# Kernel tuning notes

Measured on AMD Instinct MI355X. Metric: run time of the kernel, lower is better.

The kernel has to match this reference:

```python
import jax, jax.numpy as jnp
import numpy as np

N_NODES = 100000
N_EDGES = 1600000
IN_F = 256
OUT_F = 128


def setup_inputs() -> dict:
    key = jax.random.key(0)
    k1, k2, k3, k4, k5 = jax.random.split(key, 5)
    x = jax.random.normal(k1, (N_NODES, IN_F), dtype=jnp.float32)
    edge_rows = jax.random.randint(k2, (N_EDGES,), 0, N_NODES, dtype=jnp.int32)
    edge_cols = jax.random.randint(k3, (N_EDGES,), 0, N_NODES, dtype=jnp.int32)
    edge_vals = jax.random.uniform(k4, (N_EDGES,), dtype=jnp.float32)
    # glorot init for weight, zeros for bias (matches reset_parameters)
    limit = float(np.sqrt(6.0 / (IN_F + OUT_F)))
    weight = jax.random.uniform(k5, (IN_F, OUT_F), dtype=jnp.float32,
                                minval=-limit, maxval=limit)
    bias = jnp.zeros((OUT_F,), dtype=jnp.float32)
    return {"x": x, "edge_rows": edge_rows, "edge_cols": edge_cols,
            "edge_vals": edge_vals, "weight": weight, "bias": bias}


def reference(x, edge_rows, edge_cols, edge_vals, weight, bias):
    # dense projection: [N, in] @ [in, out] -> [N, out]
    h = x @ weight
    # spmm(adj, h): out[r] = sum_{edges e with row r} vals[e] * h[col[e]]
    msgs = edge_vals[:, None] * h[edge_cols]          # [E, out]
    agg = jax.ops.segment_sum(msgs, edge_rows, num_segments=N_NODES)
    return agg + bias
```

## Files before the change

kernel.cpp:

```cpp
#include <hip/hip_runtime.h>


typedef __attribute__((ext_vector_type(8))) short short8;
typedef __attribute__((ext_vector_type(4))) float floatx4;
typedef __attribute__((ext_vector_type(2))) int intv2;

#define WT_K 264
#define GM_NODES 128
#define BSHIFT 6
#define BROWS 64
#define CAP 192
#define CSH 4
#define OVFCAP 65536
#define XCC_GETREG_IMM 6164

static __device__ __forceinline__ uint f2bf(float x) {
  uint u = __float_as_uint(x);
  return (u + 0x7fffu + ((u >> 16) & 1u)) >> 16;
}

__global__ __launch_bounds__(256) void conv_w(const float* __restrict__ w,
                                              ushort* __restrict__ wt,
                                              int* __restrict__ cursors,
                                              int n_ints) {
  const int f = blockIdx.x;
  const int k = threadIdx.x;
  wt[f * WT_K + k] = (ushort)f2bf(w[k * 128 + f]);
  for (int i = blockIdx.x * 256 + threadIdx.x; i < n_ints; i += 128 * 256)
    cursors[i] = 0;
}

__global__ __launch_bounds__(256) void gemm_mfma(const float* __restrict__ x,
                                                 const ushort* __restrict__ wt,
                                                 ushort* __restrict__ h,
                                                 int n_nodes) {
  __shared__ ushort lw[128 * WT_K];
  __shared__ ushort xa[GM_NODES * 40];
  const int t = threadIdx.x;
  const int lane = t & 63;
  const int wq = t >> 6;
  const int quad = lane >> 4;
  const int l15 = lane & 15;
  const int row0 = blockIdx.x * GM_NODES;

  {
    const uint4* src = (const uint4*)wt;
    uint4* dst = (uint4*)lw;
    for (int i = t; i < (128 * WT_K * 2) / 16; i += 256) dst[i] = src[i];
  }

  floatx4 acc[2][8];
#pragma unroll
  for (int nt = 0; nt < 2; ++nt)
#pragma unroll
    for (int mt = 0; mt < 8; ++mt) acc[nt][mt] = (floatx4){0.f, 0.f, 0.f, 0.f};

  float4 cur[4];
#pragma unroll
  for (int i = 0; i < 4; ++i) {
    const int idx = i * 256 + t;
    const int row = idx >> 3, kq = idx & 7;
    const int gr = row0 + row;
    cur[i] = (gr < n_nodes) ? *(const float4*)&x[(size_t)gr * 256 + kq * 4]
                            : make_float4(0.f, 0.f, 0.f, 0.f);
  }

  for (int kc = 0; kc < 8; ++kc) {
#pragma unroll
    for (int i = 0; i < 4; ++i) {
      const int idx = i * 256 + t;
      const int row = idx >> 3, kq = idx & 7;
      uint2 p;
      p.x = f2bf(cur[i].x) | (f2bf(cur[i].y) << 16);
      p.y = f2bf(cur[i].z) | (f2bf(cur[i].w) << 16);
      *(uint2*)&xa[row * 40 + kq * 4] = p;
    }
    __syncthreads();

    float4 nxt[4];
    if (kc < 7) {
#pragma unroll
      for (int i = 0; i < 4; ++i) {
        const int idx = i * 256 + t;
        const int row = idx >> 3, kq = idx & 7;
        const int gr = row0 + row;
        nxt[i] = (gr < n_nodes)
                     ? *(const float4*)&x[(size_t)gr * 256 + (kc + 1) * 32 + kq * 4]
                     : make_float4(0.f, 0.f, 0.f, 0.f);
      }
    }

    short8 bfr[2];
    bfr[0] = *(const short8*)&xa[(wq * 32 + l15) * 40 + quad * 8];
    bfr[1] = *(const short8*)&xa[(wq * 32 + 16 + l15) * 40 + quad * 8];
#pragma unroll
    for (int mt = 0; mt < 8; ++mt) {
      const short8 afr =
          *(const short8*)&lw[(mt * 16 + l15) * WT_K + kc * 32 + quad * 8];
      acc[0][mt] = __builtin_amdgcn_mfma_f32_16x16x32_bf16(afr, bfr[0],
                                                           acc[0][mt], 0, 0, 0);
      acc[1][mt] = __builtin_amdgcn_mfma_f32_16x16x32_bf16(afr, bfr[1],
                                                           acc[1][mt], 0, 0, 0);
    }
    __syncthreads();
#pragma unroll
    for (int i = 0; i < 4; ++i) cur[i] = nxt[i];
  }

#pragma unroll
  for (int nt = 0; nt < 2; ++nt) {
    const int node = row0 + wq * 32 + nt * 16 + l15;
    if (node < n_nodes) {
#pragma unroll
      for (int mt = 0; mt < 8; ++mt) {
        uint2 p;
        p.x = f2bf(acc[nt][mt][0]) | (f2bf(acc[nt][mt][1]) << 16);
        p.y = f2bf(acc[nt][mt][2]) | (f2bf(acc[nt][mt][3]) << 16);
        *(uint2*)&h[(size_t)node * 128 + mt * 16 + quad * 4] = p;
      }
    }
  }
}

__global__ __launch_bounds__(256) void fill_xcd(
    const int* __restrict__ erows, const int* __restrict__ ecols,
    const float* __restrict__ evals, int* __restrict__ cursors,
    int2* __restrict__ bcv, int* __restrict__ ovf_cnt,
    int4* __restrict__ ovf, int n_edges, int nb) {
  const int base = blockIdx.x * 1024 + threadIdx.x;
  const int xcd = (int)(__builtin_amdgcn_s_getreg(XCC_GETREG_IMM)) & 7;
  int rr[4], cc[4];
  float vv[4];
#pragma unroll
  for (int j = 0; j < 4; ++j) {
    const int i = base + j * 256;
    if (i < n_edges) {
      rr[j] = __builtin_nontemporal_load(&erows[i]);
      cc[j] = __builtin_nontemporal_load(&ecols[i]);
      vv[j] = __builtin_nontemporal_load(&evals[i]);
    }
  }
#pragma unroll
  for (int j = 0; j < 4; ++j) {
    const int i = base + j * 256;
    if (i >= n_edges) continue;
    const int reg = xcd * nb + (rr[j] >> BSHIFT);
    const int pos = atomicAdd(&cursors[reg << CSH], 1);
    if (pos < CAP) {
      int2 p;
      p.x = cc[j] | ((rr[j] & (BROWS - 1)) << 17);
      p.y = __float_as_int(vv[j]);
      bcv[(size_t)reg * CAP + pos] = p;
    } else {
      int op = atomicAdd(ovf_cnt, 1);
      if (op < OVFCAP) {
        int4 q; q.x = rr[j]; q.y = cc[j]; q.z = __float_as_int(vv[j]); q.w = 0;
        ovf[op] = q;
      }
    }
  }
}

__global__ __launch_bounds__(256) void sort_gather(
    const ushort* __restrict__ h, const int* __restrict__ cursors,
    const int2* __restrict__ bcv, const float* __restrict__ bias,
    float* __restrict__ out, int n_nodes, int nb) {
  __shared__ int2 buf[8 * CAP];
  __shared__ int cnt[BROWS], start[BROWS], cur[BROWS];
  __shared__ int scnt[8];
  const int b = blockIdx.x;
  const int t = threadIdx.x;
  if (t < 8) scnt[t] = min(cursors[(t * nb + b) << CSH], CAP);
  if (t < BROWS) cnt[t] = 0;
  __syncthreads();

#pragma unroll
  for (int x = 0; x < 8; ++x) {
    const int n = scnt[x];
    const int2* src = &bcv[(size_t)(x * nb + b) * CAP];
    for (int i = t; i < n; i += 256) atomicAdd(&cnt[((uint)src[i].x) >> 17], 1);
  }
  __syncthreads();

  if (t < BROWS) {
    int c = cnt[t];
    int s = c;
#pragma unroll
    for (int off = 1; off < 64; off <<= 1) {
      int u = __shfl_up(s, off, 64);
      if (t >= off) s += u;
    }
    start[t] = s - c;
    cur[t] = s - c;
  }
  __syncthreads();

#pragma unroll
  for (int x = 0; x < 8; ++x) {
    const int n = scnt[x];
    const intv2* src = (const intv2*)&bcv[(size_t)(x * nb + b) * CAP];
    for (int i = t; i < n; i += 256) {
      intv2 rr = __builtin_nontemporal_load(&src[i]);
      int2 rec; rec.x = rr[0]; rec.y = rr[1];
      int pos = atomicAdd(&cur[((uint)rec.x) >> 17], 1);
      buf[pos] = rec;
    }
  }
  __syncthreads();

  const int lane = t & 63;
  const int w = t >> 6;
  const float2 bv = ((const float2*)bias)[lane];
  for (int rr = w * 16; rr < w * 16 + 16; ++rr) {
    const int node = b * BROWS + rr;
    if (node >= n_nodes) break;
    float2 acca = bv;
    float2 accb = make_float2(0.f, 0.f);
    int p = start[rr];
    const int p1 = start[rr] + cnt[rr];
    for (; p + 8 <= p1; p += 8) {
      int2 e0 = buf[p + 0];
      int2 e1 = buf[p + 1];
      int2 e2 = buf[p + 2];
      int2 e3 = buf[p + 3];
      int2 e4 = buf[p + 4];
      int2 e5 = buf[p + 5];
      int2 e6 = buf[p + 6];
      int2 e7 = buf[p + 7];
      uint u0 = ((const uint*)(h + (size_t)(e0.x & 0x1FFFF) * 128))[lane];
      uint u1 = ((const uint*)(h + (size_t)(e1.x & 0x1FFFF) * 128))[lane];
      uint u2 = ((const uint*)(h + (size_t)(e2.x & 0x1FFFF) * 128))[lane];
      uint u3 = ((const uint*)(h + (size_t)(e3.x & 0x1FFFF) * 128))[lane];
      uint u4 = ((const uint*)(h + (size_t)(e4.x & 0x1FFFF) * 128))[lane];
      uint u5 = ((const uint*)(h + (size_t)(e5.x & 0x1FFFF) * 128))[lane];
      uint u6 = ((const uint*)(h + (size_t)(e6.x & 0x1FFFF) * 128))[lane];
      uint u7 = ((const uint*)(h + (size_t)(e7.x & 0x1FFFF) * 128))[lane];
      float v0 = __int_as_float(e0.y), v1 = __int_as_float(e1.y);
      float v2 = __int_as_float(e2.y), v3 = __int_as_float(e3.y);
      float v4 = __int_as_float(e4.y), v5 = __int_as_float(e5.y);
      float v6 = __int_as_float(e6.y), v7 = __int_as_float(e7.y);
      acca.x += v0 * __uint_as_float(u0 << 16);
      acca.y += v0 * __uint_as_float(u0 & 0xffff0000u);
      accb.x += v1 * __uint_as_float(u1 << 16);
      accb.y += v1 * __uint_as_float(u1 & 0xffff0000u);
      acca.x += v2 * __uint_as_float(u2 << 16);
      acca.y += v2 * __uint_as_float(u2 & 0xffff0000u);
      accb.x += v3 * __uint_as_float(u3 << 16);
      accb.y += v3 * __uint_as_float(u3 & 0xffff0000u);
      acca.x += v4 * __uint_as_float(u4 << 16);
      acca.y += v4 * __uint_as_float(u4 & 0xffff0000u);
      accb.x += v5 * __uint_as_float(u5 << 16);
      accb.y += v5 * __uint_as_float(u5 & 0xffff0000u);
      acca.x += v6 * __uint_as_float(u6 << 16);
      acca.y += v6 * __uint_as_float(u6 & 0xffff0000u);
      accb.x += v7 * __uint_as_float(u7 << 16);
      accb.y += v7 * __uint_as_float(u7 & 0xffff0000u);
    }
    for (; p < p1; ++p) {
      int2 ev = buf[p];
      float v = __int_as_float(ev.y);
      uint u = ((const uint*)(h + (size_t)(ev.x & 0x1FFFF) * 128))[lane];
      acca.x += v * __uint_as_float(u << 16);
      acca.y += v * __uint_as_float(u & 0xffff0000u);
    }
    float2 accf;
    accf.x = acca.x + accb.x;
    accf.y = acca.y + accb.y;
    ((float2*)(out + (size_t)node * 128))[lane] = accf;
  }
}

__global__ __launch_bounds__(256) void ovf_scatter(
    const ushort* __restrict__ h, const int* __restrict__ ovf_cnt,
    const int4* __restrict__ ovf, float* __restrict__ out) {
  const int n = min(*ovf_cnt, OVFCAP);
  const int lane = threadIdx.x & 63;
  const int wid = (blockIdx.x * 256 + threadIdx.x) >> 6;
  const int nw = gridDim.x * 4;
  for (int e = wid; e < n; e += nw) {
    int4 rec = ovf[e];
    float v = __int_as_float(rec.z);
    uint u = ((const uint*)(h + (size_t)rec.y * 128))[lane];
    float* op = out + (size_t)rec.x * 128 + lane * 2;
    atomicAdd(op, v * __uint_as_float(u << 16));
    atomicAdd(op + 1, v * __uint_as_float(u & 0xffff0000u));
  }
}

__global__ __launch_bounds__(256) void init_bias(float* __restrict__ out,
                                                 const float* __restrict__ bias,
                                                 int n4) {
  int i = blockIdx.x * 256 + threadIdx.x;
  if (i < n4) {
    float4 b = ((const float4*)bias)[i & 31];
    ((float4*)out)[i] = b;
  }
}

__global__ __launch_bounds__(256) void scatter_edges(
    const ushort* __restrict__ h, const int* __restrict__ erows,
    const int* __restrict__ ecols, const float* __restrict__ evals,
    float* __restrict__ out, int n_edges) {
  int e = blockIdx.x * 4 + (threadIdx.x >> 6);
  if (e >= n_edges) return;
  int lane = threadIdx.x & 63;
  int row = erows[e];
  int col = ecols[e];
  float v = evals[e];
  uint u = ((const uint*)(h + (size_t)col * 128))[lane];
  float* op = out + (size_t)row * 128 + lane * 2;
  atomicAdd(op, v * __uint_as_float(u << 16));
  atomicAdd(op + 1, v * __uint_as_float(u & 0xffff0000u));
}

extern "C" void kernel_launch(void* const* d_in, const int* in_sizes, int n_in,
                              void* d_out, int out_size, void* d_ws, size_t ws_size,
                              hipStream_t stream) {
  const float* x     = (const float*)d_in[0];
  const int*   erows = (const int*)d_in[1];
  const int*   ecols = (const int*)d_in[2];
  const float* evals = (const float*)d_in[3];
  const float* w     = (const float*)d_in[4];
  const float* bias  = (const float*)d_in[5];
  float* out = (float*)d_out;

  const int n_nodes = in_sizes[0] / 256;
  const int n_edges = in_sizes[1];
  const int nb_buckets = (n_nodes + BROWS - 1) >> BSHIFT;
  const int nb8 = nb_buckets * 8;

  char* ws = (char*)d_ws;
  size_t off = 0;
  ushort* h  = (ushort*)(ws + off);  off += ((size_t)n_nodes * 128 * 2 + 255) & ~255ull;
  ushort* wt = (ushort*)(ws + off);  off += ((size_t)128 * WT_K * 2 + 255) & ~255ull;
  const size_t cur_ints = (((size_t)nb8) << CSH) + 16;
  int* cursors = (int*)(ws + off);   off += (cur_ints * 4 + 255) & ~255ull;
  int2* bcv    = (int2*)(ws + off);  off += ((size_t)nb8 * CAP * 8 + 255) & ~255ull;
  int4* ovf    = (int4*)(ws + off);  off += (size_t)OVFCAP * 16;
  const bool bucket_ok = (off <= ws_size) && (n_nodes <= (1 << 17));
  int* ovf_cnt = cursors + (((size_t)nb8) << CSH);

  const int zero_ints = bucket_ok ? (int)cur_ints : 0;
  conv_w<<<128, 256, 0, stream>>>(w, wt, cursors, zero_ints);
  const int gemm_blocks = (n_nodes + GM_NODES - 1) / GM_NODES;
  gemm_mfma<<<gemm_blocks, 256, 0, stream>>>(x, wt, h, n_nodes);

  if (bucket_ok) {
    const int eblocks = (n_edges + 1023) / 1024;
    fill_xcd<<<eblocks, 256, 0, stream>>>(erows, ecols, evals, cursors, bcv,
                                          ovf_cnt, ovf, n_edges, nb_buckets);
    sort_gather<<<nb_buckets, 256, 0, stream>>>(h, cursors, bcv, bias, out,
                                                n_nodes, nb_buckets);
    ovf_scatter<<<32, 256, 0, stream>>>(h, ovf_cnt, ovf, out);
  } else {
    const int n4 = out_size / 4;
    init_bias<<<(n4 + 255) / 256, 256, 0, stream>>>(out, bias, n4);
    scatter_edges<<<(n_edges + 3) / 4, 256, 0, stream>>>(h, erows, ecols, evals,
                                                         out, n_edges);
  }
}
```

Baseline: 334.6 us.

## Pre-bin edges in shared memory per block before global bucket reservation

Replaces the per-edge global atomic bucket fill, which used per-XCD bucket copies, with a block-local counting sort. Each block loads 6400 edges into LDS, histograms them by bucket, reserves one contiguous range per bucket with a single global atomic, then scatters the records. Buckets become unified, each holding up to 1280 records, so sort_gather reads one segment per bucket instead of eight. This cuts global atomic traffic heavily. In exchange it uses a large LDS footprint per block and adds tighter limits on node count.

```diff
diff --git a/kernel.cpp b/kernel.cpp
--- a/kernel.cpp
+++ b/kernel.cpp
@@ -9,10 +9,11 @@
 #define GM_NODES 128
 #define BSHIFT 6
 #define BROWS 64
-#define CAP 192
+#define CAP 1280
+#define NBMAX 1600
+#define EPB 6400
 #define CSH 4
 #define OVFCAP 65536
-#define XCC_GETREG_IMM 6164
 
 static __device__ __forceinline__ uint f2bf(float x) {
   uint u = __float_as_uint(x);
@@ -122,39 +123,82 @@
   }
 }
 
-__global__ __launch_bounds__(256) void fill_xcd(
+__global__ __launch_bounds__(256) void fill_bin(
     const int* __restrict__ erows, const int* __restrict__ ecols,
     const float* __restrict__ evals, int* __restrict__ cursors,
     int2* __restrict__ bcv, int* __restrict__ ovf_cnt,
     int4* __restrict__ ovf, int n_edges, int nb) {
-  const int base = blockIdx.x * 1024 + threadIdx.x;
-  const int xcd = (int)(__builtin_amdgcn_s_getreg(XCC_GETREG_IMM)) & 7;
-  int rr[4], cc[4];
-  float vv[4];
-#pragma unroll
-  for (int j = 0; j < 4; ++j) {
-    const int i = base + j * 256;
-    if (i < n_edges) {
-      rr[j] = __builtin_nontemporal_load(&erows[i]);
-      cc[j] = __builtin_nontemporal_load(&ecols[i]);
-      vv[j] = __builtin_nontemporal_load(&evals[i]);
-    }
-  }
-#pragma unroll
-  for (int j = 0; j < 4; ++j) {
-    const int i = base + j * 256;
-    if (i >= n_edges) continue;
-    const int reg = xcd * nb + (rr[j] >> BSHIFT);
-    const int pos = atomicAdd(&cursors[reg << CSH], 1);
+  __shared__ int2 rec[EPB];
+  __shared__ short bkt[EPB];
+  __shared__ int cnt[NBMAX], bas[NBMAX], cur[NBMAX];
+  const int t = threadIdx.x;
+  const int e0 = blockIdx.x * EPB;
+  const int n = min(EPB, n_edges - e0);
+  if (n <= 0) return;
+
+  for (int b = t; b < nb; b += 256) { cnt[b] = 0; cur[b] = 0; }
+  __syncthreads();
+
+  {
+    int i = t;
+    for (; i + 768 < n; i += 1024) {
+      int r0 = __builtin_nontemporal_load(&erows[e0 + i]);
+      int r1 = __builtin_nontemporal_load(&erows[e0 + i + 256]);
+      int r2 = __builtin_nontemporal_load(&erows[e0 + i + 512]);
+      int r3 = __builtin_nontemporal_load(&erows[e0 + i + 768]);
+      int c0 = __builtin_nontemporal_load(&ecols[e0 + i]);
+      int c1 = __builtin_nontemporal_load(&ecols[e0 + i + 256]);
+      int c2 = __builtin_nontemporal_load(&ecols[e0 + i + 512]);
+      int c3 = __builtin_nontemporal_load(&ecols[e0 + i + 768]);
+      float v0 = __builtin_nontemporal_load(&evals[e0 + i]);
+      float v1 = __builtin_nontemporal_load(&evals[e0 + i + 256]);
+      float v2 = __builtin_nontemporal_load(&evals[e0 + i + 512]);
+      float v3 = __builtin_nontemporal_load(&evals[e0 + i + 768]);
+      int2 p0; p0.x = c0 | ((r0 & (BROWS - 1)) << 17); p0.y = __float_as_int(v0);
+      int2 p1; p1.x = c1 | ((r1 & (BROWS - 1)) << 17); p1.y = __float_as_int(v1);
+      int2 p2; p2.x = c2 | ((r2 & (BROWS - 1)) << 17); p2.y = __float_as_int(v2);
+      int2 p3; p3.x = c3 | ((r3 & (BROWS - 1)) << 17); p3.y = __float_as_int(v3);
+      rec[i] = p0; rec[i + 256] = p1; rec[i + 512] = p2; rec[i + 768] = p3;
+      const int b0 = r0 >> BSHIFT, b1 = r1 >> BSHIFT;
+      const int b2 = r2 >> BSHIFT, b3 = r3 >> BSHIFT;
+      bkt[i] = (short)b0; bkt[i + 256] = (short)b1;
+      bkt[i + 512] = (short)b2; bkt[i + 768] = (short)b3;
+      atomicAdd(&cnt[b0], 1); atomicAdd(&cnt[b1], 1);
+      atomicAdd(&cnt[b2], 1); atomicAdd(&cnt[b3], 1);
+    }
+    for (; i < n; i += 256) {
+      const int r = __builtin_nontemporal_load(&erows[e0 + i]);
+      const int c = __builtin_nontemporal_load(&ecols[e0 + i]);
+      const float v = __builtin_nontemporal_load(&evals[e0 + i]);
+      int2 p; p.x = c | ((r & (BROWS - 1)) << 17); p.y = __float_as_int(v);
+      rec[i] = p;
+      const int b = r >> BSHIFT;
+      bkt[i] = (short)b;
+      atomicAdd(&cnt[b], 1);
+    }
+  }
+  __syncthreads();
+
+  for (int b = t; b < nb; b += 256) {
+    const int c = cnt[b];
+    if (c > 0) bas[b] = atomicAdd(&cursors[b << CSH], c);
+  }
+  __syncthreads();
+
+  for (int i = t; i < n; i += 256) {
+    const int b = (int)bkt[i];
+    const int loc = atomicAdd(&cur[b], 1);
+    const int pos = bas[b] + loc;
+    const int2 p = rec[i];
     if (pos < CAP) {
-      int2 p;
-      p.x = cc[j] | ((rr[j] & (BROWS - 1)) << 17);
-      p.y = __float_as_int(vv[j]);
-      bcv[(size_t)reg * CAP + pos] = p;
+      bcv[(size_t)b * CAP + pos] = p;
     } else {
       int op = atomicAdd(ovf_cnt, 1);
       if (op < OVFCAP) {
-        int4 q; q.x = rr[j]; q.y = cc[j]; q.z = __float_as_int(vv[j]); q.w = 0;
+        int4 q;
+        q.x = (b << BSHIFT) | ((p.x >> 17) & (BROWS - 1));
+        q.y = p.x & 0x1FFFF;
+        q.z = p.y; q.w = 0;
         ovf[op] = q;
       }
     }
@@ -165,21 +209,16 @@
     const ushort* __restrict__ h, const int* __restrict__ cursors,
     const int2* __restrict__ bcv, const float* __restrict__ bias,
     float* __restrict__ out, int n_nodes, int nb) {
-  __shared__ int2 buf[8 * CAP];
+  __shared__ int2 buf[CAP];
   __shared__ int cnt[BROWS], start[BROWS], cur[BROWS];
-  __shared__ int scnt[8];
   const int b = blockIdx.x;
   const int t = threadIdx.x;
-  if (t < 8) scnt[t] = min(cursors[(t * nb + b) << CSH], CAP);
+  const int nrec = min(cursors[b << CSH], CAP);
   if (t < BROWS) cnt[t] = 0;
   __syncthreads();
 
-#pragma unroll
-  for (int x = 0; x < 8; ++x) {
-    const int n = scnt[x];
-    const int2* src = &bcv[(size_t)(x * nb + b) * CAP];
-    for (int i = t; i < n; i += 256) atomicAdd(&cnt[((uint)src[i].x) >> 17], 1);
-  }
+  const int2* src = &bcv[(size_t)b * CAP];
+  for (int i = t; i < nrec; i += 256) atomicAdd(&cnt[((uint)src[i].x) >> 17], 1);
   __syncthreads();
 
   if (t < BROWS) {
@@ -195,16 +234,11 @@
   }
   __syncthreads();
 
-#pragma unroll
-  for (int x = 0; x < 8; ++x) {
-    const int n = scnt[x];
-    const intv2* src = (const intv2*)&bcv[(size_t)(x * nb + b) * CAP];
-    for (int i = t; i < n; i += 256) {
-      intv2 rr = __builtin_nontemporal_load(&src[i]);
-      int2 rec; rec.x = rr[0]; rec.y = rr[1];
-      int pos = atomicAdd(&cur[((uint)rec.x) >> 17], 1);
-      buf[pos] = rec;
-    }
+  for (int i = t; i < nrec; i += 256) {
+    intv2 rr = __builtin_nontemporal_load((const intv2*)&src[i]);
+    int2 recv; recv.x = rr[0]; recv.y = rr[1];
+    int pos = atomicAdd(&cur[((uint)recv.x) >> 17], 1);
+    buf[pos] = recv;
   }
   __syncthreads();
 
@@ -278,10 +312,10 @@
   const int wid = (blockIdx.x * 256 + threadIdx.x) >> 6;
   const int nw = gridDim.x * 4;
   for (int e = wid; e < n; e += nw) {
-    int4 rec = ovf[e];
-    float v = __int_as_float(rec.z);
-    uint u = ((const uint*)(h + (size_t)rec.y * 128))[lane];
-    float* op = out + (size_t)rec.x * 128 + lane * 2;
+    int4 recq = ovf[e];
+    float v = __int_as_float(recq.z);
+    uint u = ((const uint*)(h + (size_t)recq.y * 128))[lane];
+    float* op = out + (size_t)recq.x * 128 + lane * 2;
     atomicAdd(op, v * __uint_as_float(u << 16));
     atomicAdd(op + 1, v * __uint_as_float(u & 0xffff0000u));
   }
@@ -327,18 +361,18 @@
   const int n_nodes = in_sizes[0] / 256;
   const int n_edges = in_sizes[1];
   const int nb_buckets = (n_nodes + BROWS - 1) >> BSHIFT;
-  const int nb8 = nb_buckets * 8;
 
   char* ws = (char*)d_ws;
   size_t off = 0;
   ushort* h  = (ushort*)(ws + off);  off += ((size_t)n_nodes * 128 * 2 + 255) & ~255ull;
   ushort* wt = (ushort*)(ws + off);  off += ((size_t)128 * WT_K * 2 + 255) & ~255ull;
-  const size_t cur_ints = (((size_t)nb8) << CSH) + 16;
+  const size_t cur_ints = (((size_t)nb_buckets) << CSH) + 16;
   int* cursors = (int*)(ws + off);   off += (cur_ints * 4 + 255) & ~255ull;
-  int2* bcv    = (int2*)(ws + off);  off += ((size_t)nb8 * CAP * 8 + 255) & ~255ull;
+  int2* bcv    = (int2*)(ws + off);  off += ((size_t)nb_buckets * CAP * 8 + 255) & ~255ull;
   int4* ovf    = (int4*)(ws + off);  off += (size_t)OVFCAP * 16;
-  const bool bucket_ok = (off <= ws_size) && (n_nodes <= (1 << 17));
-  int* ovf_cnt = cursors + (((size_t)nb8) << CSH);
+  const bool bucket_ok = (off <= ws_size) && (nb_buckets <= NBMAX) &&
+                         (n_nodes <= 102400);
+  int* ovf_cnt = cursors + (((size_t)nb_buckets) << CSH);
 
   const int zero_ints = bucket_ok ? (int)cur_ints : 0;
   conv_w<<<128, 256, 0, stream>>>(w, wt, cursors, zero_ints);
@@ -346,8 +380,8 @@
   gemm_mfma<<<gemm_blocks, 256, 0, stream>>>(x, wt, h, n_nodes);
 
   if (bucket_ok) {
-    const int eblocks = (n_edges + 1023) / 1024;
-    fill_xcd<<<eblocks, 256, 0, stream>>>(erows, ecols, evals, cursors, bcv,
+    const int eblocks = (n_edges + EPB - 1) / EPB;
+    fill_bin<<<eblocks, 256, 0, stream>>>(erows, ecols, evals, cursors, bcv,
                                           ovf_cnt, ovf, n_edges, nb_buckets);
     sort_gather<<<nb_buckets, 256, 0, stream>>>(h, cursors, bcv, bias, out,
                                                 n_nodes, nb_buckets);
```

New measurement: 302.5 us. -9.6%, faster.
